# Kernel tuning notes

Hardware: AMD Instinct MI355X
Metric: run time of the kernel (lower is better)

Reference implementation:

```python
import jax, jax.numpy as jnp
import numpy as np

B, S, V, E = 64, 32, 50000, 300
H, D = 16, 16            # head_num, head_dim; model dim M = H*D = 256
M = H * D
AH = 200                 # attn_hidden_dim


def setup_inputs() -> dict:
    key = jax.random.key(0)
    ks = jax.random.split(key, 16)
    f = jnp.float32
    inp = {
        "x": jax.random.randint(ks[0], (B, S), 0, V),
        "emb": jax.random.normal(ks[1], (V, E), f) * 0.05,
        "W_proj": jax.random.normal(ks[2], (E, M), f) * 0.05,
        "b_proj": jnp.zeros((M,), f),
        "Wq": jax.random.normal(ks[3], (M, M), f) * 0.05,
        "bq": jnp.zeros((M,), f),
        "Wk": jax.random.normal(ks[4], (M, M), f) * 0.05,
        "bk": jnp.zeros((M,), f),
        "Wv": jax.random.normal(ks[5], (M, M), f) * 0.05,
        "bv": jnp.zeros((M,), f),
        "W_attn": jax.random.normal(ks[6], (2 * D, AH), f) * 0.05,  # attn_fc: 2*head_dim -> AH
        "b_attn": jnp.zeros((AH,), f),
        "attn_v": jax.random.normal(ks[7], (AH,), f),
        "W_fc": jax.random.normal(ks[8], (S * D, M), f) * 0.05,     # lazy fc: context.size(-1)=S*D -> M
        "b_fc": jnp.zeros((M,), f),
    }
    return inp


def reference(x, emb, W_proj, b_proj, Wq, bq, Wk, bk, Wv, bv,
              W_attn, b_attn, attn_v, W_fc, b_fc):
    # embedding + projection (300 -> 256); dropout = identity (eval)
    h = emb[x]                                   # [B,S,E]
    h = h @ W_proj + b_proj                      # [B,S,M]

    q = (h @ Wq + bq).reshape(B, S, H, D)        # [B,S,H,D]
    k = (h @ Wk + bk).reshape(B, S, H, D)
    v = (h @ Wv + bv).reshape(B, S, H, D)

    # attn_fc(concat(q_i, k_j)) = q_i @ W1 + k_j @ W2 + b  (exact same math, no concat)
    W1, W2 = W_attn[:D], W_attn[D:]              # each [D,AH]
    aq = jnp.einsum('bihd,de->bihe', q, W1)      # [B,S,H,AH]
    ak = jnp.einsum('bjhd,de->bjhe', k, W2)      # [B,S,H,AH]
    hid = jnp.tanh(aq[:, :, None] + ak[:, None, :] + b_attn)   # [B,S,S,H,AH]
    scores = jnp.einsum('bijhe,e->bijh', hid, attn_v)          # [B,S,S,H]

    w = jax.nn.softmax(scores, axis=2)           # softmax over key dim (dim=2)

    # torch.matmul([B,S,S,H], [B,S,H,D]) -> [B,S,S,D]: heads contracted, v at QUERY pos
    ctx = jnp.einsum('bijh,bihd->bijd', w, v)    # [B,S,S,D]
    ctx = ctx.reshape(B, S, S * D)               # [B,S,S*D]

    out = ctx @ W_fc + b_fc                      # [B,S,M]
    return out.max(axis=1)                       # AdaptiveMaxPool1d(1) over seq -> [B,M]
```

## Files before the change

kernel.cpp:

```cpp
#include <hip/hip_runtime.h>

#define B 64
#define S 32
#define V 50000
#define E 300
#define H 16
#define D 16
#define M 256
#define AH 200
#define BS 2048

#define C2 2.88539008177793f
#define LOG2E 1.44269504088896f

#if __has_builtin(__builtin_amdgcn_exp2f)
#define EXP2(x) __builtin_amdgcn_exp2f(x)
#else
#define EXP2(x) __builtin_exp2f(x)
#endif

__global__ __launch_bounds__(1024) void k1_embed_qkv(
    const int* __restrict__ x, const float* __restrict__ emb,
    const float* __restrict__ W_proj, const float* __restrict__ b_proj,
    const float* __restrict__ Wq, const float* __restrict__ bq,
    const float* __restrict__ Wk, const float* __restrict__ bk,
    const float* __restrict__ Wv, const float* __restrict__ bv,
    float* __restrict__ q, float* __restrict__ k, float* __restrict__ v)
{
    __shared__ float embl[8][E];
    __shared__ float hl[8][M];
    __shared__ float part[8][8][M];
    __shared__ int idxl[8];
    const int tid = threadIdx.x;
    const int col2 = (tid & 127) * 2;
    const int grp = tid >> 7;
    const int r0 = blockIdx.x * 8;
    const int rr = tid >> 7;
    const int rc2 = (tid & 127) * 2;

    if (tid < 8) idxl[tid] = x[r0 + tid];
    __syncthreads();
    for (int t = tid; t < 8 * E; t += 1024) {
        int r = t / E, e = t % E;
        embl[r][e] = emb[(long)idxl[r] * E + e];
    }
    __syncthreads();

    if (grp < 6) {
        float2 acc[8];
#pragma unroll
        for (int r = 0; r < 8; r++) acc[r] = make_float2(0.f, 0.f);
        const int e0 = 50 * grp;
#pragma unroll 4
        for (int e = e0; e < e0 + 50; e += 2) {
            float2 w0 = *reinterpret_cast<const float2*>(&W_proj[e * M + col2]);
            float2 w1 = *reinterpret_cast<const float2*>(&W_proj[(e + 1) * M + col2]);
#pragma unroll
            for (int r = 0; r < 8; r++) {
                float2 hm = *reinterpret_cast<const float2*>(&embl[r][e]);
                acc[r].x += hm.x * w0.x; acc[r].y += hm.x * w0.y;
                acc[r].x += hm.y * w1.x; acc[r].y += hm.y * w1.y;
            }
        }
#pragma unroll
        for (int r = 0; r < 8; r++)
            *reinterpret_cast<float2*>(&part[grp][r][col2]) = acc[r];
    }
    __syncthreads();
    {
        float2 s = *reinterpret_cast<const float2*>(&b_proj[rc2]);
#pragma unroll
        for (int g = 0; g < 6; g++) {
            float2 p = *reinterpret_cast<const float2*>(&part[g][rr][rc2]);
            s.x += p.x; s.y += p.y;
        }
        *reinterpret_cast<float2*>(&hl[rr][rc2]) = s;
    }
    __syncthreads();

    float2 aq[8], ak[8], av[8];
#pragma unroll
    for (int r = 0; r < 8; r++) {
        aq[r] = make_float2(0.f, 0.f);
        ak[r] = make_float2(0.f, 0.f);
        av[r] = make_float2(0.f, 0.f);
    }
    {
        const int cb = 32 * grp;
#pragma unroll 2
        for (int c = cb; c < cb + 32; c += 2) {
            float2 wq0 = *reinterpret_cast<const float2*>(&Wq[c * M + col2]);
            float2 wk0 = *reinterpret_cast<const float2*>(&Wk[c * M + col2]);
            float2 wv0 = *reinterpret_cast<const float2*>(&Wv[c * M + col2]);
            float2 wq1 = *reinterpret_cast<const float2*>(&Wq[(c + 1) * M + col2]);
            float2 wk1 = *reinterpret_cast<const float2*>(&Wk[(c + 1) * M + col2]);
            float2 wv1 = *reinterpret_cast<const float2*>(&Wv[(c + 1) * M + col2]);
#pragma unroll
            for (int r = 0; r < 8; r++) {
                float2 hm = *reinterpret_cast<const float2*>(&hl[r][c]);
                aq[r].x += hm.x * wq0.x; aq[r].y += hm.x * wq0.y;
                ak[r].x += hm.x * wk0.x; ak[r].y += hm.x * wk0.y;
                av[r].x += hm.x * wv0.x; av[r].y += hm.x * wv0.y;
                aq[r].x += hm.y * wq1.x; aq[r].y += hm.y * wq1.y;
                ak[r].x += hm.y * wk1.x; ak[r].y += hm.y * wk1.y;
                av[r].x += hm.y * wv1.x; av[r].y += hm.y * wv1.y;
            }
        }
    }
#pragma unroll
    for (int r = 0; r < 8; r++)
        *reinterpret_cast<float2*>(&part[grp][r][col2]) = aq[r];
    __syncthreads();
    {
        float2 s = *reinterpret_cast<const float2*>(&bq[rc2]);
#pragma unroll
        for (int g = 0; g < 8; g++) {
            float2 p = *reinterpret_cast<const float2*>(&part[g][rr][rc2]);
            s.x += p.x; s.y += p.y;
        }
        *reinterpret_cast<float2*>(&q[(r0 + rr) * M + rc2]) = s;
    }
    __syncthreads();
#pragma unroll
    for (int r = 0; r < 8; r++)
        *reinterpret_cast<float2*>(&part[grp][r][col2]) = ak[r];
    __syncthreads();
    {
        float2 s = *reinterpret_cast<const float2*>(&bk[rc2]);
#pragma unroll
        for (int g = 0; g < 8; g++) {
            float2 p = *reinterpret_cast<const float2*>(&part[g][rr][rc2]);
            s.x += p.x; s.y += p.y;
        }
        *reinterpret_cast<float2*>(&k[(r0 + rr) * M + rc2]) = s;
    }
    __syncthreads();
#pragma unroll
    for (int r = 0; r < 8; r++)
        *reinterpret_cast<float2*>(&part[grp][r][col2]) = av[r];
    __syncthreads();
    {
        float2 s = *reinterpret_cast<const float2*>(&bv[rc2]);
#pragma unroll
        for (int g = 0; g < 8; g++) {
            float2 p = *reinterpret_cast<const float2*>(&part[g][rr][rc2]);
            s.x += p.x; s.y += p.y;
        }
        *reinterpret_cast<float2*>(&v[(r0 + rr) * M + rc2]) = s;
    }
}

#define AQS 204
#define EKS 34
__global__ __launch_bounds__(512) void k2_scores(
    const float* __restrict__ q, const float* __restrict__ k,
    const float* __restrict__ W_attn, const float* __restrict__ b_attn,
    const float* __restrict__ attn_v, float* __restrict__ wout)
{
    __shared__ __align__(16) float ql[S][D];
    __shared__ __align__(16) float kl[S][D];
    __shared__ __align__(16) float Eq[S][AQS];
    __shared__ __align__(16) float Ekt[AH][EKS];
    const int tid = threadIdx.x;
    const int b = blockIdx.x / H, h = blockIdx.x % H;

    ql[tid >> 4][tid & 15] = q[(b * S + (tid >> 4)) * M + h * D + (tid & 15)];
    kl[tid >> 4][tid & 15] = k[(b * S + (tid >> 4)) * M + h * D + (tid & 15)];
    __syncthreads();

    if (tid < AH) {
        const int e = tid;
        float w1c[D];
#pragma unroll
        for (int d = 0; d < D; d++) w1c[d] = W_attn[d * AH + e];
        float be = b_attn[e];
        for (int i = 0; i < S; i++) {
            float a1 = be;
#pragma unroll
            for (int d = 0; d < D; d++) a1 += ql[i][d] * w1c[d];
            Eq[i][e] = EXP2(C2 * a1);
        }
    } else if (tid >= 256 && tid < 256 + AH) {
        const int e = tid - 256;
        float w2c[D];
#pragma unroll
        for (int d = 0; d < D; d++) w2c[d] = W_attn[(D + d) * AH + e];
        for (int j = 0; j < S; j++) {
            float a2 = 0.f;
#pragma unroll
            for (int d = 0; d < D; d++) a2 += kl[j][d] * w2c[d];
            Ekt[e][j] = EXP2(C2 * a2);
        }
    }
    __syncthreads();

    const int i = tid >> 4;
    const int j0 = tid & 15;
    float acc0 = 0.f, acc1 = 0.f;
    const float4* avp = reinterpret_cast<const float4*>(attn_v);
#pragma unroll 2
    for (int ec = 0; ec < AH / 4; ec++) {
        float4 eq = *reinterpret_cast<const float4*>(&Eq[i][4 * ec]);
        float4 avv = avp[ec];
        float2 e0 = *reinterpret_cast<const float2*>(&Ekt[4 * ec + 0][2 * j0]);
        float2 e1 = *reinterpret_cast<const float2*>(&Ekt[4 * ec + 1][2 * j0]);
        float2 e2 = *reinterpret_cast<const float2*>(&Ekt[4 * ec + 2][2 * j0]);
        float2 e3 = *reinterpret_cast<const float2*>(&Ekt[4 * ec + 3][2 * j0]);
        {
            float a0 = 1.f + eq.x * e0.x, a1 = 1.f + eq.y * e1.x;
            float a2 = 1.f + eq.z * e2.x, a3 = 1.f + eq.w * e3.x;
            float p01 = a0 * a1, p23 = a2 * a3;
            float t01 = avv.x * a1 + avv.y * a0;
            float t23 = avv.z * a3 + avv.w * a2;
            float num = t01 * p23 + t23 * p01;
            acc0 += num * __builtin_amdgcn_rcpf(p01 * p23);
        }
        {
            float a0 = 1.f + eq.x * e0.y, a1 = 1.f + eq.y * e1.y;
            float a2 = 1.f + eq.z * e2.y, a3 = 1.f + eq.w * e3.y;
            float p01 = a0 * a1, p23 = a2 * a3;
            float t01 = avv.x * a1 + avv.y * a0;
            float t23 = avv.z * a3 + avv.w * a2;
            float num = t01 * p23 + t23 * p01;
            acc1 += num * __builtin_amdgcn_rcpf(p01 * p23);
        }
    }
    float sc0 = -2.f * acc0, sc1 = -2.f * acc1;

    float mx = fmaxf(sc0, sc1);
#pragma unroll
    for (int msk = 1; msk < 16; msk <<= 1) mx = fmaxf(mx, __shfl_xor(mx, msk, 64));
    float p0 = EXP2(LOG2E * (sc0 - mx));
    float p1 = EXP2(LOG2E * (sc1 - mx));
    float ps = p0 + p1;
#pragma unroll
    for (int msk = 1; msk < 16; msk <<= 1) ps += __shfl_xor(ps, msk, 64);
    float rs = __builtin_amdgcn_rcpf(ps);

    float2 w2v = make_float2(p0 * rs, p1 * rs);
    *reinterpret_cast<float2*>(&wout[((b * H + h) * S + i) * S + 2 * j0]) = w2v;
}

__global__ __launch_bounds__(1024) void k3_ctx_fc(
    const float* __restrict__ v, const float* __restrict__ wmat,
    const float* __restrict__ W_fc, const float* __restrict__ b_fc,
    float* __restrict__ part_out)
{
    __shared__ float vl[8][H][D];
    __shared__ float wl[H][8][S];
    __shared__ float ctxl[8][S * D];
    __shared__ float pfc[4][8][M];
    const int tid = threadIdx.x;
    const int b = blockIdx.x >> 2, ig = blockIdx.x & 3;

    for (int t = tid; t < 8 * M; t += 1024) {
        int i = t >> 8, md = t & 255;
        vl[i][md >> 4][md & 15] = v[(b * S + ig * 8 + i) * M + md];
    }
    for (int t = tid; t < H * 8 * S; t += 1024) {
        int h = t >> 8, r = t & 255;
        int i = r >> 5, j = r & 31;
        wl[h][i][j] = wmat[((b * H + h) * S + (ig * 8 + i)) * S + j];
    }
    __syncthreads();

    for (int t = tid; t < 8 * S * D; t += 1024) {
        int i = t >> 9, jd = t & 511;
        int j = jd >> 4, d = jd & 15;
        float a = 0.f;
#pragma unroll
        for (int h = 0; h < H; h++) a += wl[h][i][j] * vl[i][h][d];
        ctxl[i][j * D + d] = a;
    }
    __syncthreads();

    const int col = tid & 255, grp = tid >> 8;
    {
        float acc[8];
#pragma unroll
        for (int ii = 0; ii < 8; ii++) acc[ii] = 0.f;
        const int e0 = 128 * grp;
#pragma unroll 4
        for (int e = e0; e < e0 + 128; e++) {
            float wf = W_fc[e * M + col];
#pragma unroll
            for (int ii = 0; ii < 8; ii++) acc[ii] += ctxl[ii][e] * wf;
        }
#pragma unroll
        for (int ii = 0; ii < 8; ii++) pfc[grp][ii][col] = acc[ii];
    }
    __syncthreads();
    if (tid < 256) {
        float bf = b_fc[tid];
        float mxv = -3.4e38f;
#pragma unroll
        for (int ii = 0; ii < 8; ii++) {
            float s = pfc[0][ii][tid] + pfc[1][ii][tid] + pfc[2][ii][tid]
                    + pfc[3][ii][tid] + bf;
            mxv = fmaxf(mxv, s);
        }
        part_out[(b * 4 + ig) * M + tid] = mxv;
    }
}

__global__ __launch_bounds__(256) void k4_max(
    const float* __restrict__ part, float* __restrict__ out)
{
    const int b = blockIdx.x, m = threadIdx.x;
    float v0 = part[(b * 4 + 0) * M + m];
    float v1 = part[(b * 4 + 1) * M + m];
    float v2 = part[(b * 4 + 2) * M + m];
    float v3 = part[(b * 4 + 3) * M + m];
    out[b * M + m] = fmaxf(fmaxf(v0, v1), fmaxf(v2, v3));
}

extern "C" void kernel_launch(void* const* d_in, const int* in_sizes, int n_in,
                              void* d_out, int out_size, void* d_ws, size_t ws_size,
                              hipStream_t stream) {
    const int*   x      = (const int*)  d_in[0];
    const float* emb    = (const float*)d_in[1];
    const float* W_proj = (const float*)d_in[2];
    const float* b_proj = (const float*)d_in[3];
    const float* Wq     = (const float*)d_in[4];
    const float* bq     = (const float*)d_in[5];
    const float* Wk     = (const float*)d_in[6];
    const float* bk     = (const float*)d_in[7];
    const float* Wv     = (const float*)d_in[8];
    const float* bv     = (const float*)d_in[9];
    const float* W_attn = (const float*)d_in[10];
    const float* b_attn = (const float*)d_in[11];
    const float* attn_v = (const float*)d_in[12];
    const float* W_fc   = (const float*)d_in[13];
    const float* b_fc   = (const float*)d_in[14];
    float* out = (float*)d_out;

    float* ws   = (float*)d_ws;
    float* q    = ws;
    float* k    = q + BS * M;
    float* v    = k + BS * M;
    float* wmat = v + BS * M;
    float* part = wmat + B * H * S * S;

    k1_embed_qkv<<<BS / 8, 1024, 0, stream>>>(x, emb, W_proj, b_proj,
                                              Wq, bq, Wk, bk, Wv, bv, q, k, v);
    k2_scores<<<B * H, 512, 0, stream>>>(q, k, W_attn, b_attn, attn_v, wmat);
    k3_ctx_fc<<<B * 4, 1024, 0, stream>>>(v, wmat, W_fc, b_fc, part);
    k4_max<<<B, 256, 0, stream>>>(part, out);
}
```

Measured before the change: 85.53 us.

## Split score kernel over attention-hidden halves and move softmax into ctx kernel

The scores kernel now launches twice as many blocks. Each block handles half of the 200 attention-hidden units and writes partial scores into one of two buffers. The Eq/Ek precompute now uses all four thread groups with float4 shared reads. Softmax moves into the context/FC kernel, which sums the two partial score buffers before normalizing. The intent is better occupancy and parallelism in the dominant tanh-score stage, at the cost of an extra score buffer in global memory and more reads in the third kernel.

```diff
diff --git a/kernel.cpp b/kernel.cpp
--- a/kernel.cpp
+++ b/kernel.cpp
@@ -8,6 +8,7 @@
 #define D 16
 #define M 256
 #define AH 200
+#define AHH 100
 #define BS 2048
 
 #define C2 2.88539008177793f
@@ -150,46 +151,66 @@
     }
 }
 
-#define AQS 204
+#define EQS 104
 #define EKS 34
-__global__ __launch_bounds__(512) void k2_scores(
+__global__ __launch_bounds__(512, 8) void k2_scores(
     const float* __restrict__ q, const float* __restrict__ k,
     const float* __restrict__ W_attn, const float* __restrict__ b_attn,
-    const float* __restrict__ attn_v, float* __restrict__ wout)
+    const float* __restrict__ attn_v, float* __restrict__ psc)
 {
     __shared__ __align__(16) float ql[S][D];
     __shared__ __align__(16) float kl[S][D];
-    __shared__ __align__(16) float Eq[S][AQS];
-    __shared__ __align__(16) float Ekt[AH][EKS];
+    __shared__ __align__(16) float Eqs[S][EQS];
+    __shared__ __align__(16) float Ekts[AHH][EKS];
     const int tid = threadIdx.x;
-    const int b = blockIdx.x / H, h = blockIdx.x % H;
+    const int eh = blockIdx.x & 1;
+    const int h = (blockIdx.x >> 1) & 15;
+    const int b = blockIdx.x >> 5;
+    const int e0g = eh * AHH;
 
     ql[tid >> 4][tid & 15] = q[(b * S + (tid >> 4)) * M + h * D + (tid & 15)];
     kl[tid >> 4][tid & 15] = k[(b * S + (tid >> 4)) * M + h * D + (tid & 15)];
     __syncthreads();
 
-    if (tid < AH) {
-        const int e = tid;
-        float w1c[D];
-#pragma unroll
-        for (int d = 0; d < D; d++) w1c[d] = W_attn[d * AH + e];
-        float be = b_attn[e];
-        for (int i = 0; i < S; i++) {
-            float a1 = be;
-#pragma unroll
-            for (int d = 0; d < D; d++) a1 += ql[i][d] * w1c[d];
-            Eq[i][e] = EXP2(C2 * a1);
-        }
-    } else if (tid >= 256 && tid < 256 + AH) {
-        const int e = tid - 256;
-        float w2c[D];
-#pragma unroll
-        for (int d = 0; d < D; d++) w2c[d] = W_attn[(D + d) * AH + e];
-        for (int j = 0; j < S; j++) {
-            float a2 = 0.f;
-#pragma unroll
-            for (int d = 0; d < D; d++) a2 += kl[j][d] * w2c[d];
-            Ekt[e][j] = EXP2(C2 * a2);
+    {
+        const int e = tid & 127;
+        const int pg = tid >> 7;
+        if (e < AHH) {
+            const int eg = e0g + e;
+            if (pg < 2) {
+                float w1c[D];
+#pragma unroll
+                for (int d = 0; d < D; d++) w1c[d] = W_attn[d * AH + eg];
+                float be = b_attn[eg];
+                const int i0 = pg * 16;
+                for (int i = i0; i < i0 + 16; i++) {
+                    float a1 = be;
+                    const float4* qr = reinterpret_cast<const float4*>(&ql[i][0]);
+#pragma unroll
+                    for (int dq = 0; dq < 4; dq++) {
+                        float4 qv = qr[dq];
+                        a1 += qv.x * w1c[4 * dq] + qv.y * w1c[4 * dq + 1]
+                            + qv.z * w1c[4 * dq + 2] + qv.w * w1c[4 * dq + 3];
+                    }
+                    Eqs[i][e] = EXP2(C2 * a1);
+                }
+            } else {
+                float w2c[D];
+#pragma unroll
+                for (int d = 0; d < D; d++) w2c[d] = W_attn[(D + d) * AH + eg];
+                const int j0i = (pg - 2) * 16;
+                for (int j = j0i; j < j0i + 16; j++) {
+                    float a2 = 0.f;
+                    const float4* kr = reinterpret_cast<const float4*>(&kl[j][0]);
+#pragma unroll
+                    for (int dq = 0; dq < 4; dq++) {
+                        float4 kv = kr[dq];
+                        a2 += kv.x * w2c[4 * dq] + kv.y * w2c[4 * dq + 1]
+                            + kv.z * w2c[4 * dq + 2] + kv.w * w2c[4 * dq + 3];
+                    }
+                    Ekts[e][j] = EXP2(C2 * a2);
+                }
+            }
         }
     }
     __syncthreads();
@@ -197,15 +218,15 @@
     const int i = tid >> 4;
     const int j0 = tid & 15;
     float acc0 = 0.f, acc1 = 0.f;
-    const float4* avp = reinterpret_cast<const float4*>(attn_v);
-#pragma unroll 2
-    for (int ec = 0; ec < AH / 4; ec++) {
-        float4 eq = *reinterpret_cast<const float4*>(&Eq[i][4 * ec]);
+    const float4* avp = reinterpret_cast<const float4*>(attn_v + e0g);
+#pragma unroll 1
+    for (int ec = 0; ec < AHH / 4; ec++) {
+        float4 eq = *reinterpret_cast<const float4*>(&Eqs[i][4 * ec]);
         float4 avv = avp[ec];
-        float2 e0 = *reinterpret_cast<const float2*>(&Ekt[4 * ec + 0][2 * j0]);
-        float2 e1 = *reinterpret_cast<const float2*>(&Ekt[4 * ec + 1][2 * j0]);
-        float2 e2 = *reinterpret_cast<const float2*>(&Ekt[4 * ec + 2][2 * j0]);
-        float2 e3 = *reinterpret_cast<const float2*>(&Ekt[4 * ec + 3][2 * j0]);
+        float2 e0 = *reinterpret_cast<const float2*>(&Ekts[4 * ec + 0][2 * j0]);
+        float2 e1 = *reinterpret_cast<const float2*>(&Ekts[4 * ec + 1][2 * j0]);
+        float2 e2 = *reinterpret_cast<const float2*>(&Ekts[4 * ec + 2][2 * j0]);
+        float2 e3 = *reinterpret_cast<const float2*>(&Ekts[4 * ec + 3][2 * j0]);
         {
             float a0 = 1.f + eq.x * e0.x, a1 = 1.f + eq.y * e1.x;
             float a2 = 1.f + eq.z * e2.x, a3 = 1.f + eq.w * e3.x;
@@ -225,33 +246,24 @@
             acc1 += num * __builtin_amdgcn_rcpf(p01 * p23);
         }
     }
-    float sc0 = -2.f * acc0, sc1 = -2.f * acc1;
-
-    float mx = fmaxf(sc0, sc1);
-#pragma unroll
-    for (int msk = 1; msk < 16; msk <<= 1) mx = fmaxf(mx, __shfl_xor(mx, msk, 64));
-    float p0 = EXP2(LOG2E * (sc0 - mx));
-    float p1 = EXP2(LOG2E * (sc1 - mx));
-    float ps = p0 + p1;
-#pragma unroll
-    for (int msk = 1; msk < 16; msk <<= 1) ps += __shfl_xor(ps, msk, 64);
-    float rs = __builtin_amdgcn_rcpf(ps);
-
-    float2 w2v = make_float2(p0 * rs, p1 * rs);
-    *reinterpret_cast<float2*>(&wout[((b * H + h) * S + i) * S + 2 * j0]) = w2v;
+    float2 out2 = make_float2(-2.f * acc0, -2.f * acc1);
+    float* po = psc + (size_t)eh * (B * H * S * S);
+    *reinterpret_cast<float2*>(&po[((b * H + h) * S + i) * S + 2 * j0]) = out2;
 }
 
 __global__ __launch_bounds__(1024) void k3_ctx_fc(
-    const float* __restrict__ v, const float* __restrict__ wmat,
+    const float* __restrict__ v, const float* __restrict__ psc,
     const float* __restrict__ W_fc, const float* __restrict__ b_fc,
     float* __restrict__ part_out)
 {
     __shared__ float vl[8][H][D];
-    __shared__ float wl[H][8][S];
+    __shared__ __align__(16) float wl[H][8][S];
     __shared__ float ctxl[8][S * D];
     __shared__ float pfc[4][8][M];
     const int tid = threadIdx.x;
     const int b = blockIdx.x >> 2, ig = blockIdx.x & 3;
+    const float* psc0 = psc;
+    const float* psc1 = psc + (size_t)(B * H * S * S);
 
     for (int t = tid; t < 8 * M; t += 1024) {
         int i = t >> 8, md = t & 255;
@@ -260,7 +272,29 @@
     for (int t = tid; t < H * 8 * S; t += 1024) {
         int h = t >> 8, r = t & 255;
         int i = r >> 5, j = r & 31;
-        wl[h][i][j] = wmat[((b * H + h) * S + (ig * 8 + i)) * S + j];
+        int idx = ((b * H + h) * S + (ig * 8 + i)) * S + j;
+        wl[h][i][j] = psc0[idx] + psc1[idx];
+    }
+    __syncthreads();
+
+    {
+        const int row = tid >> 3;
+        const int h = row >> 3, il = row & 7;
+        const int jq = (tid & 7) * 4;
+        float4 sv = *reinterpret_cast<const float4*>(&wl[h][il][jq]);
+        float mx = fmaxf(fmaxf(sv.x, sv.y), fmaxf(sv.z, sv.w));
+#pragma unroll
+        for (int msk = 1; msk < 8; msk <<= 1) mx = fmaxf(mx, __shfl_xor(mx, msk, 64));
+        float p0 = EXP2(LOG2E * (sv.x - mx));
+        float p1 = EXP2(LOG2E * (sv.y - mx));
+        float p2 = EXP2(LOG2E * (sv.z - mx));
+        float p3 = EXP2(LOG2E * (sv.w - mx));
+        float ps = p0 + p1 + p2 + p3;
+#pragma unroll
+        for (int msk = 1; msk < 8; msk <<= 1) ps += __shfl_xor(ps, msk, 64);
+        float rs = __builtin_amdgcn_rcpf(ps);
+        float4 wv = make_float4(p0 * rs, p1 * rs, p2 * rs, p3 * rs);
+        *reinterpret_cast<float4*>(&wl[h][il][jq]) = wv;
     }
     __syncthreads();
 
@@ -338,12 +372,12 @@
     float* q    = ws;
     float* k    = q + BS * M;
     float* v    = k + BS * M;
-    float* wmat = v + BS * M;
-    float* part = wmat + B * H * S * S;
+    float* psc  = v + BS * M;
+    float* part = psc + 2 * B * H * S * S;
 
     k1_embed_qkv<<<BS / 8, 1024, 0, stream>>>(x, emb, W_proj, b_proj,
                                               Wq, bq, Wk, bk, Wv, bv, q, k, v);
-    k2_scores<<<B * H, 512, 0, stream>>>(q, k, W_attn, b_attn, attn_v, wmat);
-    k3_ctx_fc<<<B * 4, 1024, 0, stream>>>(v, wmat, W_fc, b_fc, part);
+    k2_scores<<<B * H * 2, 512, 0, stream>>>(q, k, W_attn, b_attn, attn_v, psc);
+    k3_ctx_fc<<<B * 4, 1024, 0, stream>>>(v, psc, W_fc, b_fc, part);
     k4_max<<<B, 256, 0, stream>>>(part, out);
 }
```

Result: no change. 84.16 us (-1.6%).
